# Performance work log

Hardware: AMD Instinct MI355X
Metric: run time of the kernel (lower is better)

## Reference

```python
import jax, jax.numpy as jnp
import numpy as np

N_QUBITS = 4
N_LAYERS = 2


def _apply_rx(state, theta, wire):
    """Apply RX(theta) on `wire`. state: [B] + [2]*n complex. theta: [B] or scalar."""
    n = state.ndim - 1
    ax = wire + 1
    half = jnp.asarray(theta) * 0.5
    c = jnp.cos(half)
    s = jnp.sin(half)
    # broadcast angle over the remaining qubit axes after taking the wire slice
    c = jnp.reshape(c, c.shape + (1,) * (n - 1))
    s = jnp.reshape(s, s.shape + (1,) * (n - 1))
    s0 = jnp.take(state, 0, axis=ax)
    s1 = jnp.take(state, 1, axis=ax)
    new0 = c * s0 - 1j * s * s1
    new1 = -1j * s * s0 + c * s1
    return jnp.stack([new0, new1], axis=ax)


def _apply_cnot(state, control, target):
    cax = control + 1
    tax = target + 1
    sub0 = jnp.take(state, 0, axis=cax)
    sub1 = jnp.take(state, 1, axis=cax)
    tax_sub = tax if tax < cax else tax - 1
    sub1 = jnp.flip(sub1, axis=tax_sub)  # X on target when control == 1
    return jnp.stack([sub0, sub1], axis=cax)


def _quantum_circuit(x, w):
    """AngleEmbedding(RX) + BasicEntanglerLayers(RX + CNOT ring), PauliZ expvals.
    x: [B, n_qubits] float32 angles; w: [n_layers, n_qubits] float32.
    Returns [B, n_qubits] float32."""
    B = x.shape[0]
    n = N_QUBITS
    state = jnp.zeros((B,) + (2,) * n, dtype=jnp.complex64)
    state = state.at[(slice(None),) + (0,) * n].set(1.0)
    # AngleEmbedding: RX(x_q) on wire q (per-sample angles)
    for q in range(n):
        state = _apply_rx(state, x[:, q], q)
    # BasicEntanglerLayers: per layer, RX(w[l,q]) on each wire then CNOT ring
    for l in range(N_LAYERS):
        for q in range(n):
            state = _apply_rx(state, w[l, q], q)
        for q in range(n):
            state = _apply_cnot(state, q, (q + 1) % n)
    probs = jnp.abs(state) ** 2  # [B, 2,2,2,2]
    flat = probs.reshape(B, -1)  # [B, 16]
    # <Z_q> = sum_b p(b) * (+1 if bit q == 0 else -1)
    bits = ((jnp.arange(2 ** n)[:, None] >> (n - 1 - jnp.arange(n))[None, :]) & 1)
    signs = (1.0 - 2.0 * bits).astype(jnp.float32)  # [16, n]
    return flat @ signs  # [B, n]


def setup_inputs() -> dict:
    key = jax.random.key(0)
    ks = jax.random.split(key, 5)
    B = 65536
    inputs = jax.random.normal(ks[0], (B, 28, 28), dtype=jnp.float32)
    W1 = jax.random.normal(ks[1], (784, N_QUBITS), dtype=jnp.float32) * 0.05
    b1 = jnp.zeros((N_QUBITS,), dtype=jnp.float32)
    qw = jax.random.normal(ks[2], (N_LAYERS, N_QUBITS), dtype=jnp.float32) * 0.1
    W2 = jax.random.normal(ks[3], (N_QUBITS, 32), dtype=jnp.float32) * 0.3
    b2 = jnp.zeros((32,), dtype=jnp.float32)
    W3 = jax.random.normal(ks[4], (32, 2), dtype=jnp.float32) * 0.2
    b3 = jnp.zeros((2,), dtype=jnp.float32)
    return {"inputs": inputs, "W1": W1, "b1": b1, "qw": qw, "W2": W2, "b2": b2, "W3": W3, "b3": b3}


def reference(inputs, W1, b1, qw, W2, b2, W3, b3):
    B = inputs.shape[0]
    flat = inputs.reshape(B, -1)                      # flatten
    pre = jax.nn.relu(flat @ W1 + b1)                 # dense_preprocess [B, 4]
    q = _quantum_circuit(pre, qw)                     # [B, 4]
    q = jnp.where(jnp.isnan(q), jnp.zeros_like(q), q)
    post = jax.nn.relu(q @ W2 + b2)                   # dense_postprocess [B, 32]
    return jax.nn.softmax(post @ W3 + b3, axis=-1)    # output_layer [B, 2]
```

## Files before the change

### kernel.cpp

```cpp
#include <hip/hip_runtime.h>
#include <math.h>


constexpr int ROW  = 784;
constexpr int ROW4 = 196;

__device__ __forceinline__ void apply_rx(float (&sr)[16], float (&si)[16],
                                         int mask, float c, float s)
{
    #pragma unroll
    for (int i = 0; i < 16; i++) {
        if (!(i & mask)) {
            int j = i | mask;
            float x0 = sr[i], y0 = si[i], x1 = sr[j], y1 = si[j];
            sr[i] = fmaf(c, x0,  s * y1);
            si[i] = fmaf(c, y0, -s * x1);
            sr[j] = fmaf(c, x1,  s * y0);
            si[j] = fmaf(c, y1, -s * x0);
        }
    }
}

__device__ __forceinline__ void apply_cnot(float (&sr)[16], float (&si)[16],
                                           int cmask, int tmask)
{
    #pragma unroll
    for (int i = 0; i < 16; i++) {
        if ((i & cmask) && !(i & tmask)) {
            int j = i | tmask;
            float tr = sr[i]; sr[i] = sr[j]; sr[j] = tr;
            float ti = si[i]; si[i] = si[j]; si[j] = ti;
        }
    }
}

#define FMA_ONE(xv, wrow, o0) \
    a[(o0)+0] = fmaf(xv, wrow.x, a[(o0)+0]); \
    a[(o0)+1] = fmaf(xv, wrow.y, a[(o0)+1]); \
    a[(o0)+2] = fmaf(xv, wrow.z, a[(o0)+2]); \
    a[(o0)+3] = fmaf(xv, wrow.w, a[(o0)+3]);

#define FMA_ROUND(xb, o0, o1) { \
    _Pragma("unroll") \
    for (int i = 0; i < 4; i++) { \
        FMA_ONE(xb[i].x,     w[i][0], o0) FMA_ONE(xb[4+i].x, w[i][0], o1) \
        FMA_ONE(xb[i].y,     w[i][1], o0) FMA_ONE(xb[4+i].y, w[i][1], o1) \
        FMA_ONE(xb[i].z,     w[i][2], o0) FMA_ONE(xb[4+i].z, w[i][2], o1) \
        FMA_ONE(xb[i].w,     w[i][3], o0) FMA_ONE(xb[4+i].w, w[i][3], o1) \
    } }

#define LOAD_ROUND(dst, sA, sB) { \
    const float4* p0_ = X4 + (size_t)(sA) * ROW4; \
    const float4* p1_ = X4 + (size_t)(sB) * ROW4; \
    dst[0] = p0_[lane];        dst[4] = p1_[lane]; \
    dst[1] = p0_[lane + 64];   dst[5] = p1_[lane + 64]; \
    dst[2] = p0_[lane + 128];  dst[6] = p1_[lane + 128]; \
    dst[3] = tail ? p0_[192 + lane] : zero4; \
    dst[7] = tail ? p1_[192 + lane] : zero4; }

__global__ __launch_bounds__(256) void fused_kernel(
    const float* __restrict__ X,
    const float* __restrict__ W1,
    const float* __restrict__ b1,
    const float* __restrict__ qw,
    const float* __restrict__ W2,
    const float* __restrict__ b2,
    const float* __restrict__ W3,
    const float* __restrict__ b3,
    float* __restrict__ out,
    int B)
{
    const int lane = threadIdx.x & 63;
    const int wid  = (blockIdx.x * 256 + threadIdx.x) >> 6;
    const int nW   = (gridDim.x * 256) >> 6;
    const bool tail = (lane < 4);
    const int  jt   = 192 + (lane & 3);

    const float4* X4   = reinterpret_cast<const float4*>(X);
    const float4* W1f4 = reinterpret_cast<const float4*>(W1);

    float4 w[4][4];
    #pragma unroll
    for (int i = 0; i < 4; i++) {
        const int j4 = (i < 3) ? (lane + (i << 6)) : jt;
        #pragma unroll
        for (int p = 0; p < 4; p++) w[i][p] = W1f4[4 * j4 + p];
    }

    const int idx = ((lane >> 5) & 1) * 16 + ((lane >> 4) & 1) * 8 +
                    ((lane >> 3) & 1) * 4  + ((lane >> 2) & 1) * 2 +
                    ((lane >> 1) & 1);
    const float bl = b1[idx & 3];

    const bool b5  = (lane & 32) != 0;
    const bool b4  = (lane & 16) != 0;
    const bool b3f = (lane & 8)  != 0;
    const bool b2f = (lane & 4)  != 0;
    const bool b1f = (lane & 2)  != 0;

    const float4 zero4 = make_float4(0.f, 0.f, 0.f, 0.f);
    const int sl = B - 1;

    for (int S = wid * 8; S < B; S += nW * 8) {
        const int s0 = (S     < sl) ? S     : sl;
        const int s1 = (S + 1 < sl) ? S + 1 : sl;
        const int s2 = (S + 2 < sl) ? S + 2 : sl;
        const int s3 = (S + 3 < sl) ? S + 3 : sl;
        const int s4 = (S + 4 < sl) ? S + 4 : sl;
        const int s5 = (S + 5 < sl) ? S + 5 : sl;
        const int s6 = (S + 6 < sl) ? S + 6 : sl;
        const int s7 = (S + 7 < sl) ? S + 7 : sl;

        float a[32];
        #pragma unroll
        for (int i = 0; i < 32; i++) a[i] = 0.f;

        float4 xA[8], xB[8];
        LOAD_ROUND(xA, s0, s1)
        LOAD_ROUND(xB, s2, s3)
        FMA_ROUND(xA, 0, 4)
        LOAD_ROUND(xA, s4, s5)
        FMA_ROUND(xB, 8, 12)
        LOAD_ROUND(xB, s6, s7)
        FMA_ROUND(xA, 16, 20)
        FMA_ROUND(xB, 24, 28)

        float v16[16];
        #pragma unroll
        for (int i = 0; i < 16; i++) {
            float kv = b5 ? a[i + 16] : a[i];
            float sv = b5 ? a[i]      : a[i + 16];
            v16[i] = kv + __shfl_xor(sv, 32);
        }
        float v8a[8];
        #pragma unroll
        for (int i = 0; i < 8; i++) {
            float kv = b4 ? v16[i + 8] : v16[i];
            float sv = b4 ? v16[i]     : v16[i + 8];
            v8a[i] = kv + __shfl_xor(sv, 16);
        }
        float v4a[4];
        #pragma unroll
        for (int i = 0; i < 4; i++) {
            float kv = b3f ? v8a[i + 4] : v8a[i];
            float sv = b3f ? v8a[i]     : v8a[i + 4];
            v4a[i] = kv + __shfl_xor(sv, 8);
        }
        float v2a[2];
        #pragma unroll
        for (int i = 0; i < 2; i++) {
            float kv = b2f ? v4a[i + 2] : v4a[i];
            float sv = b2f ? v4a[i]     : v4a[i + 2];
            v2a[i] = kv + __shfl_xor(sv, 4);
        }
        float kv = b1f ? v2a[1] : v2a[0];
        float sv = b1f ? v2a[0] : v2a[1];
        float v1 = kv + __shfl_xor(sv, 2);
        v1 += __shfl_xor(v1, 1);

        const float pre_val = fmaxf(v1 + bl, 0.f);

        const float p0 = __shfl(pre_val, ((lane & 7) << 3) + 0);
        const float p1 = __shfl(pre_val, ((lane & 7) << 3) + 2);
        const float p2 = __shfl(pre_val, ((lane & 7) << 3) + 4);
        const float p3 = __shfl(pre_val, ((lane & 7) << 3) + 6);

        if (lane < 8 && S + lane < B) {
            const int s = S + lane;

            float sr[16], si[16];
            #pragma unroll
            for (int i = 0; i < 16; i++) { sr[i] = 0.f; si[i] = 0.f; }
            sr[0] = 1.f;

            {
                float c, sn;
                __sincosf(p0 * 0.5f, &sn, &c); apply_rx(sr, si, 8, c, sn);
                __sincosf(p1 * 0.5f, &sn, &c); apply_rx(sr, si, 4, c, sn);
                __sincosf(p2 * 0.5f, &sn, &c); apply_rx(sr, si, 2, c, sn);
                __sincosf(p3 * 0.5f, &sn, &c); apply_rx(sr, si, 1, c, sn);
            }

            #pragma unroll
            for (int l = 0; l < 2; l++) {
                #pragma unroll
                for (int q = 0; q < 4; q++) {
                    float c, sn;
                    __sincosf(qw[l * 4 + q] * 0.5f, &sn, &c);
                    apply_rx(sr, si, 8 >> q, c, sn);
                }
                apply_cnot(sr, si, 8, 4);
                apply_cnot(sr, si, 4, 2);
                apply_cnot(sr, si, 2, 1);
                apply_cnot(sr, si, 1, 8);
            }

            float z0 = 0.f, z1 = 0.f, z2 = 0.f, z3 = 0.f;
            #pragma unroll
            for (int i = 0; i < 16; i++) {
                float p = fmaf(sr[i], sr[i], si[i] * si[i]);
                z0 += (i & 8) ? -p : p;
                z1 += (i & 4) ? -p : p;
                z2 += (i & 2) ? -p : p;
                z3 += (i & 1) ? -p : p;
            }
            z0 = (z0 == z0) ? z0 : 0.f;
            z1 = (z1 == z1) ? z1 : 0.f;
            z2 = (z2 == z2) ? z2 : 0.f;
            z3 = (z3 == z3) ? z3 : 0.f;

            float l0 = b3[0], l1 = b3[1];
            #pragma unroll
            for (int k = 0; k < 32; k++) {
                float v = b2[k];
                v = fmaf(z0, W2[k],      v);
                v = fmaf(z1, W2[32 + k], v);
                v = fmaf(z2, W2[64 + k], v);
                v = fmaf(z3, W2[96 + k], v);
                v = fmaxf(v, 0.f);
                l0 = fmaf(v, W3[2 * k],     l0);
                l1 = fmaf(v, W3[2 * k + 1], l1);
            }

            float m  = fmaxf(l0, l1);
            float e0 = __expf(l0 - m), e1 = __expf(l1 - m);
            float inv = 1.f / (e0 + e1);
            reinterpret_cast<float2*>(out)[s] = make_float2(e0 * inv, e1 * inv);
        }
    }
}

extern "C" void kernel_launch(void* const* d_in, const int* in_sizes, int n_in,
                              void* d_out, int out_size, void* d_ws, size_t ws_size,
                              hipStream_t stream)
{
    const float* X  = (const float*)d_in[0];
    const float* W1 = (const float*)d_in[1];
    const float* b1 = (const float*)d_in[2];
    const float* qw = (const float*)d_in[3];
    const float* W2 = (const float*)d_in[4];
    const float* b2 = (const float*)d_in[5];
    const float* W3 = (const float*)d_in[6];
    const float* b3 = (const float*)d_in[7];

    const int B = in_sizes[0] / ROW;

    fused_kernel<<<2048, 256, 0, stream>>>(X, W1, b1, qw, W2, b2, W3, b3,
                                           (float*)d_out, B);
}
```

Baseline: 293.0 us.

## Prefetch next batch rows across loop iterations and hoist quantum weight trig

Restructures the persistent loop so the first two row-pair loads for the next 8-sample group are issued during the current group's FMA and reduction/quantum tail. This hides global load latency across iterations. The sincos of the fixed circuit weights moves out of the per-sample path into registers. The grid shrinks from 2048 to 512 blocks, so each wave handles more groups and the prefetch has more iterations to work over. In exchange, register pressure rises from the live prefetch buffers and there is less occupancy to hide latency with.

```diff
diff --git a/kernel.cpp b/kernel.cpp
--- a/kernel.cpp
+++ b/kernel.cpp
@@ -57,6 +57,8 @@
     dst[2] = p0_[lane + 128];  dst[6] = p1_[lane + 128]; \
     dst[3] = tail ? p0_[192 + lane] : zero4; \
     dst[7] = tail ? p1_[192 + lane] : zero4; }
+
+#define CLMP(v) (((v) < sl) ? (v) : sl)
 
 __global__ __launch_bounds__(256) void fused_kernel(
     const float* __restrict__ X,
@@ -87,6 +89,10 @@
         for (int p = 0; p < 4; p++) w[i][p] = W1f4[4 * j4 + p];
     }
 
+    float qc[8], qs[8];
+    #pragma unroll
+    for (int i = 0; i < 8; i++) __sincosf(qw[i] * 0.5f, &qs[i], &qc[i]);
+
     const int idx = ((lane >> 5) & 1) * 16 + ((lane >> 4) & 1) * 8 +
                     ((lane >> 3) & 1) * 4  + ((lane >> 2) & 1) * 2 +
                     ((lane >> 1) & 1);
@@ -99,31 +105,32 @@
     const bool b1f = (lane & 2)  != 0;
 
     const float4 zero4 = make_float4(0.f, 0.f, 0.f, 0.f);
-    const int sl = B - 1;
-
-    for (int S = wid * 8; S < B; S += nW * 8) {
-        const int s0 = (S     < sl) ? S     : sl;
-        const int s1 = (S + 1 < sl) ? S + 1 : sl;
-        const int s2 = (S + 2 < sl) ? S + 2 : sl;
-        const int s3 = (S + 3 < sl) ? S + 3 : sl;
-        const int s4 = (S + 4 < sl) ? S + 4 : sl;
-        const int s5 = (S + 5 < sl) ? S + 5 : sl;
-        const int s6 = (S + 6 < sl) ? S + 6 : sl;
-        const int s7 = (S + 7 < sl) ? S + 7 : sl;
+    const int sl   = B - 1;
+    const int step = nW * 8;
+
+    int S = wid * 8;
+    if (S >= B) return;
+
+    float4 xA[8], xB[8];
+    LOAD_ROUND(xA, CLMP(S),     CLMP(S + 1))
+    LOAD_ROUND(xB, CLMP(S + 2), CLMP(S + 3))
+
+    for (;;) {
+        const int  Sn   = S + step;
+        const bool more = (Sn < B);
 
         float a[32];
         #pragma unroll
         for (int i = 0; i < 32; i++) a[i] = 0.f;
 
-        float4 xA[8], xB[8];
-        LOAD_ROUND(xA, s0, s1)
-        LOAD_ROUND(xB, s2, s3)
         FMA_ROUND(xA, 0, 4)
-        LOAD_ROUND(xA, s4, s5)
+        LOAD_ROUND(xA, CLMP(S + 4), CLMP(S + 5))
         FMA_ROUND(xB, 8, 12)
-        LOAD_ROUND(xB, s6, s7)
+        LOAD_ROUND(xB, CLMP(S + 6), CLMP(S + 7))
         FMA_ROUND(xA, 16, 20)
+        if (more) LOAD_ROUND(xA, CLMP(Sn), CLMP(Sn + 1))
         FMA_ROUND(xB, 24, 28)
+        if (more) LOAD_ROUND(xB, CLMP(Sn + 2), CLMP(Sn + 3))
 
         float v16[16];
         #pragma unroll
@@ -184,11 +191,8 @@
             #pragma unroll
             for (int l = 0; l < 2; l++) {
                 #pragma unroll
-                for (int q = 0; q < 4; q++) {
-                    float c, sn;
-                    __sincosf(qw[l * 4 + q] * 0.5f, &sn, &c);
-                    apply_rx(sr, si, 8 >> q, c, sn);
-                }
+                for (int q = 0; q < 4; q++)
+                    apply_rx(sr, si, 8 >> q, qc[l * 4 + q], qs[l * 4 + q]);
                 apply_cnot(sr, si, 8, 4);
                 apply_cnot(sr, si, 4, 2);
                 apply_cnot(sr, si, 2, 1);
@@ -227,6 +231,9 @@
             float inv = 1.f / (e0 + e1);
             reinterpret_cast<float2*>(out)[s] = make_float2(e0 * inv, e1 * inv);
         }
+
+        if (!more) break;
+        S = Sn;
     }
 }
 
@@ -245,6 +252,6 @@
 
     const int B = in_sizes[0] / ROW;
 
-    fused_kernel<<<2048, 256, 0, stream>>>(X, W1, b1, qw, W2, b2, W3, b3,
-                                           (float*)d_out, B);
-}
+    fused_kernel<<<512, 256, 0, stream>>>(X, W1, b1, qw, W2, b2, W3, b3,
+                                          (float*)d_out, B);
+}
```

Measured after the change: 308.8 us. 5.4% more time.

## Batch 32 samples per wave with cross-iteration prefetch and lane-parallel circuit

Applied to the files above, without the earlier changes.

Each wave now handles 32 consecutive samples in four unrolled 8-sample rounds. Loads for the next round are issued before the current round's FMAs finish, so memory latency is software-pipelined across rounds. The pre-activations are gathered so the quantum circuit and MLP tail run once on 32 lanes instead of four times on 8 lanes, cutting divergent serial tail work. The grid is sized to B/128 blocks instead of a fixed grid-stride loop, which raises register pressure and drops the persistent-loop structure.

```diff
diff --git a/kernel.cpp b/kernel.cpp
--- a/kernel.cpp
+++ b/kernel.cpp
@@ -57,6 +57,8 @@
     dst[2] = p0_[lane + 128];  dst[6] = p1_[lane + 128]; \
     dst[3] = tail ? p0_[192 + lane] : zero4; \
     dst[7] = tail ? p1_[192 + lane] : zero4; }
+
+#define CLMP(v) (((v) < sl) ? (v) : sl)
 
 __global__ __launch_bounds__(256) void fused_kernel(
     const float* __restrict__ X,
@@ -72,7 +74,6 @@
 {
     const int lane = threadIdx.x & 63;
     const int wid  = (blockIdx.x * 256 + threadIdx.x) >> 6;
-    const int nW   = (gridDim.x * 256) >> 6;
     const bool tail = (lane < 4);
     const int  jt   = 192 + (lane & 3);
 
@@ -101,29 +102,31 @@
     const float4 zero4 = make_float4(0.f, 0.f, 0.f, 0.f);
     const int sl = B - 1;
 
-    for (int S = wid * 8; S < B; S += nW * 8) {
-        const int s0 = (S     < sl) ? S     : sl;
-        const int s1 = (S + 1 < sl) ? S + 1 : sl;
-        const int s2 = (S + 2 < sl) ? S + 2 : sl;
-        const int s3 = (S + 3 < sl) ? S + 3 : sl;
-        const int s4 = (S + 4 < sl) ? S + 4 : sl;
-        const int s5 = (S + 5 < sl) ? S + 5 : sl;
-        const int s6 = (S + 6 < sl) ? S + 6 : sl;
-        const int s7 = (S + 7 < sl) ? S + 7 : sl;
+    const int S = wid * 32;
+    if (S >= B) return;
+
+    float p0 = 0.f, p1 = 0.f, p2 = 0.f, p3 = 0.f;
+
+    float4 xA[8], xB[8];
+    LOAD_ROUND(xA, CLMP(S),     CLMP(S + 1))
+    LOAD_ROUND(xB, CLMP(S + 2), CLMP(S + 3))
+
+    #pragma unroll
+    for (int it = 0; it < 4; it++) {
+        const int Sb = S + it * 8;
 
         float a[32];
         #pragma unroll
         for (int i = 0; i < 32; i++) a[i] = 0.f;
 
-        float4 xA[8], xB[8];
-        LOAD_ROUND(xA, s0, s1)
-        LOAD_ROUND(xB, s2, s3)
         FMA_ROUND(xA, 0, 4)
-        LOAD_ROUND(xA, s4, s5)
+        LOAD_ROUND(xA, CLMP(Sb + 4), CLMP(Sb + 5))
         FMA_ROUND(xB, 8, 12)
-        LOAD_ROUND(xB, s6, s7)
+        LOAD_ROUND(xB, CLMP(Sb + 6), CLMP(Sb + 7))
         FMA_ROUND(xA, 16, 20)
+        if (it < 3) LOAD_ROUND(xA, CLMP(Sb + 8), CLMP(Sb + 9))
         FMA_ROUND(xB, 24, 28)
+        if (it < 3) LOAD_ROUND(xB, CLMP(Sb + 10), CLMP(Sb + 11))
 
         float v16[16];
         #pragma unroll
@@ -160,73 +163,74 @@
 
         const float pre_val = fmaxf(v1 + bl, 0.f);
 
-        const float p0 = __shfl(pre_val, ((lane & 7) << 3) + 0);
-        const float p1 = __shfl(pre_val, ((lane & 7) << 3) + 2);
-        const float p2 = __shfl(pre_val, ((lane & 7) << 3) + 4);
-        const float p3 = __shfl(pre_val, ((lane & 7) << 3) + 6);
-
-        if (lane < 8 && S + lane < B) {
-            const int s = S + lane;
-
-            float sr[16], si[16];
+        const float g0 = __shfl(pre_val, ((lane & 7) << 3) + 0);
+        const float g1 = __shfl(pre_val, ((lane & 7) << 3) + 2);
+        const float g2 = __shfl(pre_val, ((lane & 7) << 3) + 4);
+        const float g3 = __shfl(pre_val, ((lane & 7) << 3) + 6);
+        if ((lane >> 3) == it) { p0 = g0; p1 = g1; p2 = g2; p3 = g3; }
+    }
+
+    if (lane < 32 && S + lane < B) {
+        const int s = S + lane;
+
+        float sr[16], si[16];
+        #pragma unroll
+        for (int i = 0; i < 16; i++) { sr[i] = 0.f; si[i] = 0.f; }
+        sr[0] = 1.f;
+
+        {
+            float c, sn;
+            __sincosf(p0 * 0.5f, &sn, &c); apply_rx(sr, si, 8, c, sn);
+            __sincosf(p1 * 0.5f, &sn, &c); apply_rx(sr, si, 4, c, sn);
+            __sincosf(p2 * 0.5f, &sn, &c); apply_rx(sr, si, 2, c, sn);
+            __sincosf(p3 * 0.5f, &sn, &c); apply_rx(sr, si, 1, c, sn);
+        }
+
+        #pragma unroll
+        for (int l = 0; l < 2; l++) {
             #pragma unroll
-            for (int i = 0; i < 16; i++) { sr[i] = 0.f; si[i] = 0.f; }
-            sr[0] = 1.f;
-
-            {
+            for (int q = 0; q < 4; q++) {
                 float c, sn;
-                __sincosf(p0 * 0.5f, &sn, &c); apply_rx(sr, si, 8, c, sn);
-                __sincosf(p1 * 0.5f, &sn, &c); apply_rx(sr, si, 4, c, sn);
-                __sincosf(p2 * 0.5f, &sn, &c); apply_rx(sr, si, 2, c, sn);
-                __sincosf(p3 * 0.5f, &sn, &c); apply_rx(sr, si, 1, c, sn);
+                __sincosf(qw[l * 4 + q] * 0.5f, &sn, &c);
+                apply_rx(sr, si, 8 >> q, c, sn);
             }
-
-            #pragma unroll
-            for (int l = 0; l < 2; l++) {
-                #pragma unroll
-                for (int q = 0; q < 4; q++) {
-                    float c, sn;
-                    __sincosf(qw[l * 4 + q] * 0.5f, &sn, &c);
-                    apply_rx(sr, si, 8 >> q, c, sn);
-                }
-                apply_cnot(sr, si, 8, 4);
-                apply_cnot(sr, si, 4, 2);
-                apply_cnot(sr, si, 2, 1);
-                apply_cnot(sr, si, 1, 8);
-            }
-
-            float z0 = 0.f, z1 = 0.f, z2 = 0.f, z3 = 0.f;
-            #pragma unroll
-            for (int i = 0; i < 16; i++) {
-                float p = fmaf(sr[i], sr[i], si[i] * si[i]);
-                z0 += (i & 8) ? -p : p;
-                z1 += (i & 4) ? -p : p;
-                z2 += (i & 2) ? -p : p;
-                z3 += (i & 1) ? -p : p;
-            }
-            z0 = (z0 == z0) ? z0 : 0.f;
-            z1 = (z1 == z1) ? z1 : 0.f;
-            z2 = (z2 == z2) ? z2 : 0.f;
-            z3 = (z3 == z3) ? z3 : 0.f;
-
-            float l0 = b3[0], l1 = b3[1];
-            #pragma unroll
-            for (int k = 0; k < 32; k++) {
-                float v = b2[k];
-                v = fmaf(z0, W2[k],      v);
-                v = fmaf(z1, W2[32 + k], v);
-                v = fmaf(z2, W2[64 + k], v);
-                v = fmaf(z3, W2[96 + k], v);
-                v = fmaxf(v, 0.f);
-                l0 = fmaf(v, W3[2 * k],     l0);
-                l1 = fmaf(v, W3[2 * k + 1], l1);
-            }
-
-            float m  = fmaxf(l0, l1);
-            float e0 = __expf(l0 - m), e1 = __expf(l1 - m);
-            float inv = 1.f / (e0 + e1);
-            reinterpret_cast<float2*>(out)[s] = make_float2(e0 * inv, e1 * inv);
-        }
+            apply_cnot(sr, si, 8, 4);
+            apply_cnot(sr, si, 4, 2);
+            apply_cnot(sr, si, 2, 1);
+            apply_cnot(sr, si, 1, 8);
+        }
+
+        float z0 = 0.f, z1 = 0.f, z2 = 0.f, z3 = 0.f;
+        #pragma unroll
+        for (int i = 0; i < 16; i++) {
+            float p = fmaf(sr[i], sr[i], si[i] * si[i]);
+            z0 += (i & 8) ? -p : p;
+            z1 += (i & 4) ? -p : p;
+            z2 += (i & 2) ? -p : p;
+            z3 += (i & 1) ? -p : p;
+        }
+        z0 = (z0 == z0) ? z0 : 0.f;
+        z1 = (z1 == z1) ? z1 : 0.f;
+        z2 = (z2 == z2) ? z2 : 0.f;
+        z3 = (z3 == z3) ? z3 : 0.f;
+
+        float l0 = b3[0], l1 = b3[1];
+        #pragma unroll
+        for (int k = 0; k < 32; k++) {
+            float v = b2[k];
+            v = fmaf(z0, W2[k],      v);
+            v = fmaf(z1, W2[32 + k], v);
+            v = fmaf(z2, W2[64 + k], v);
+            v = fmaf(z3, W2[96 + k], v);
+            v = fmaxf(v, 0.f);
+            l0 = fmaf(v, W3[2 * k],     l0);
+            l1 = fmaf(v, W3[2 * k + 1], l1);
+        }
+
+        float m  = fmaxf(l0, l1);
+        float e0 = __expf(l0 - m), e1 = __expf(l1 - m);
+        float inv = 1.f / (e0 + e1);
+        reinterpret_cast<float2*>(out)[s] = make_float2(e0 * inv, e1 * inv);
     }
 }
 
@@ -245,6 +249,7 @@
 
     const int B = in_sizes[0] / ROW;
 
-    fused_kernel<<<2048, 256, 0, stream>>>(X, W1, b1, qw, W2, b2, W3, b3,
-                                           (float*)d_out, B);
-}
+    const int blocks = (B + 127) / 128;
+    fused_kernel<<<blocks, 256, 0, stream>>>(X, W1, b1, qw, W2, b2, W3, b3,
+                                             (float*)d_out, B);
+}
```

After: 294.4 us. No clear change (+0.5%).
